# Kernel optimization log

Measured on AMD Instinct MI355X. Metric: run time of the kernel, lower is better.

## Reference

```python
import jax, jax.numpy as jnp
import numpy as np

NUM_BLOCKS = 8
WIDTH = 512
HIDDEN_SIZE_FACTOR = 1
HARD_THRESH_FRAC = 1.0
BLOCK_SIZE = WIDTH // NUM_BLOCKS


def setup_inputs() -> dict:
    key = jax.random.key(0)
    k_x, k1, k2, k3, k4 = jax.random.split(key, 5)
    B, L, P, C = 4, 2048, WIDTH, 8
    bs = BLOCK_SIZE
    hf = HIDDEN_SIZE_FACTOR
    scale = 1.0 / (bs * bs * hf)
    x = jax.random.normal(k_x, (B, L, P, C), dtype=jnp.float32)
    w1 = scale * jax.random.uniform(k1, (2, NUM_BLOCKS, bs, bs * hf), dtype=jnp.float32)
    b1 = scale * jax.random.uniform(k2, (2, NUM_BLOCKS, bs * hf), dtype=jnp.float32)
    w2 = scale * jax.random.uniform(k3, (2, NUM_BLOCKS, bs * hf, bs), dtype=jnp.float32)
    b2 = scale * jax.random.uniform(k4, (2, NUM_BLOCKS, bs), dtype=jnp.float32)
    return {"x": x, "w1": w1, "b1": b1, "w2": w2, "b2": b2}


def _gelu(v):
    # torch nn.GELU default is the exact (erf) variant
    return jax.nn.gelu(v, approximate=False)


def reference(x, w1, b1, w2, b2):
    B, L, P, C = x.shape
    nb, bs = NUM_BLOCKS, BLOCK_SIZE
    # rfft along L (norm='ortho'); complex64
    xf = jnp.fft.rfft(x, axis=1, norm="ortho")          # (B, Lf, P, C)
    Lf = xf.shape[1]
    xf = jnp.transpose(xf, (0, 1, 3, 2))                  # (B, Lf, C, P)
    xf = xf.reshape(B, Lf, C, nb, bs)                     # split P into blocks
    kept = int(Lf * HARD_THRESH_FRAC)
    xr, xi = jnp.real(xf[:, :kept]), jnp.imag(xf[:, :kept])
    # block-diagonal complex 2-layer MLP
    mm = lambda a, w: jnp.einsum("blcni,nio->blcno", a, w)
    o1r = _gelu(mm(xr, w1[0]) - mm(xi, w1[1]) + b1[0])
    o1i = _gelu(mm(xi, w1[0]) + mm(xr, w1[1]) + b1[1])
    o2r = mm(o1r, w2[0]) - mm(o1i, w2[1]) + b2[0]
    o2i = mm(o1i, w2[0]) + mm(o1r, w2[1]) + b2[1]
    # zero-pad the thresholded modes (no-op when kept == Lf)
    pad = Lf - kept
    if pad > 0:
        z = jnp.zeros((B, pad, C, nb, bs), dtype=o2r.dtype)
        o2r = jnp.concatenate([o2r, z], axis=1)
        o2i = jnp.concatenate([o2i, z], axis=1)
    xc = (o2r + 1j * o2i).reshape(B, Lf, C, P)
    out = jnp.fft.irfft(xc, n=L, axis=1, norm="ortho")  # (B, L, C, P)
    out = jnp.transpose(out, (0, 1, 3, 2))               # (B, L, P, C)
    return (out + x).astype(x.dtype)
```

## Files before the change

### kernel.cpp

```cpp
#include <hip/hip_runtime.h>
#include <hip/hip_bf16.h>

typedef unsigned short u16;
typedef unsigned int   u32;
typedef __bf16 bf16x8 __attribute__((ext_vector_type(8)));
typedef float  f32x4  __attribute__((ext_vector_type(4)));
typedef u32    u32x2  __attribute__((ext_vector_type(2)));

#define KPAD 1088
#define SEQ  1104
#define PI_F 3.14159265358979323846f
#define WAVE_FENCE() asm volatile("s_waitcnt lgkmcnt(0)" ::: "memory")

__device__ __forceinline__ u16 f2bf(float f){
    u32 u = __float_as_uint(f);
    return (u16)((u + 0x7FFFu + ((u >> 16) & 1u)) >> 16);
}
__device__ __forceinline__ float bf2f(u16 v){ return __uint_as_float(((u32)v) << 16); }
__device__ __forceinline__ int zmap2(int e){ return e + (e >> 4) + 4*(e >> 8); }

__device__ __forceinline__ int sig(int k){
    k &= 1023;
    int a = (k >> 6) + (((k >> 2) & 15) << 4) + ((k & 3) << 8);
    return zmap2(a);
}

__device__ __forceinline__ float2 cmul(float2 a, float2 b){
    return make_float2(a.x*b.x - a.y*b.y, a.x*b.y + a.y*b.x);
}
__device__ __forceinline__ void fft4v(float2& x0, float2& x1, float2& x2, float2& x3){
    float2 t0 = make_float2(x0.x+x2.x, x0.y+x2.y);
    float2 t1 = make_float2(x0.x-x2.x, x0.y-x2.y);
    float2 t2 = make_float2(x1.x+x3.x, x1.y+x3.y);
    float2 t3 = make_float2(x1.x-x3.x, x1.y-x3.y);
    x0 = make_float2(t0.x+t2.x, t0.y+t2.y);
    x2 = make_float2(t0.x-t2.x, t0.y-t2.y);
    x1 = make_float2(t1.x+t3.y, t1.y-t3.x);
    x3 = make_float2(t1.x-t3.y, t1.y+t3.x);
}
__device__ __forceinline__ void fft16(float2 a[16]){
    #pragma unroll
    for (int u1 = 0; u1 < 4; ++u1) fft4v(a[u1], a[u1+4], a[u1+8], a[u1+12]);
    const float Cq = 0.70710678118654752f;
    const float c1 = 0.92387953251128674f, s1 = 0.38268343236508977f;
    a[5]  = cmul(a[5],  make_float2(c1, -s1));
    a[6]  = cmul(a[6],  make_float2(Cq, -Cq));
    a[7]  = cmul(a[7],  make_float2(s1, -c1));
    a[9]  = cmul(a[9],  make_float2(Cq, -Cq));
    a[10] = cmul(a[10], make_float2(0.0f, -1.0f));
    a[11] = cmul(a[11], make_float2(-Cq, -Cq));
    a[13] = cmul(a[13], make_float2(s1, -c1));
    a[14] = cmul(a[14], make_float2(-Cq, -Cq));
    a[15] = cmul(a[15], make_float2(-c1, s1));
    #pragma unroll
    for (int ja = 0; ja < 4; ++ja) fft4v(a[4*ja], a[4*ja+1], a[4*ja+2], a[4*ja+3]);
}

__device__ __forceinline__ void fft_stepA_wave(float2* Z, int lane){
    #pragma unroll
    for (int i = 0; i < 4; ++i){
        int q = lane + 64*i;
        int u = (q >> 4) & 15;
        float s_, c_;
        __sincosf(-2.0f*PI_F*(float)u*(1.0f/64.0f), &s_, &c_);
        float2 tw1 = make_float2(c_, s_);
        float2 tw2 = cmul(tw1, tw1);
        float2 tw3 = cmul(tw2, tw1);
        float2 x0 = Z[zmap2(q)], x1 = Z[zmap2(q+256)], x2 = Z[zmap2(q+512)], x3 = Z[zmap2(q+768)];
        fft4v(x0, x1, x2, x3);
        Z[zmap2(q)]     = x0;
        Z[zmap2(q+256)] = cmul(x1, tw1);
        Z[zmap2(q+512)] = cmul(x2, tw2);
        Z[zmap2(q+768)] = cmul(x3, tw3);
    }
}
__device__ __forceinline__ void fft_stepB_wave(float2* Z, int lane){
    int nA = lane & 15, jv = lane >> 4;
    float2 a[16];
    #pragma unroll
    for (int u = 0; u < 16; ++u) a[u] = Z[zmap2(nA + 16*u + 256*jv)];
    fft16(a);
    float s_, c_;
    __sincosf(-2.0f*PI_F*(float)(nA*jv)*(1.0f/1024.0f), &s_, &c_);
    float2 tw = make_float2(c_, s_);
    __sincosf(-2.0f*PI_F*(float)nA*(1.0f/256.0f), &s_, &c_);
    float2 st = make_float2(c_, s_);
    #pragma unroll
    for (int ju = 0; ju < 16; ++ju){
        Z[zmap2(nA + 16*ju + 256*jv)] = cmul(a[((ju&3)<<2)|(ju>>2)], tw);
        tw = cmul(tw, st);
    }
}
__device__ __forceinline__ void fft_stepC_wave(float2* Z, int lane){
    int ju = (lane & 63) >> 2, jv = lane & 3;
    float2 a[16];
    #pragma unroll
    for (int nA = 0; nA < 16; ++nA) a[nA] = Z[zmap2(nA + 16*ju + 256*jv)];
    fft16(a);
    #pragma unroll
    for (int kO = 0; kO < 16; ++kO)
        Z[zmap2(kO + 16*ju + 256*jv)] = a[((kO&3)<<2)|(kO>>2)];
}

__global__ __launch_bounds__(256) void prep_w(const float* __restrict__ w1,
                                              const float* __restrict__ w2,
                                              u16* __restrict__ WSW){
    int gid = blockIdx.x * 256 + threadIdx.x;
    int qd = gid >> 12;
    int t  = qd & 1;
    int n  = (qd >> 1) & 7;
    int l  = qd >> 4;
    int rr = gid & 4095;
    int o  = rr >> 6;
    int k  = rr & 63;
    const float* w = l ? w2 : w1;
    WSW[gid] = f2bf(w[((size_t)(t*8 + n)*64 + k)*64 + o]);
}


__device__ __forceinline__ u16 unpack_one(const float2* Zc, int k, int pl, float sf){
    float2 Zk = Zc[sig(k)], Zm = Zc[sig(1024 - k)];
    float sn_, cs_; __sincosf(PI_F*(float)k*(1.0f/1024.0f), &sn_, &cs_);
    float Er=0.5f*(Zk.x+Zm.x), Ei=0.5f*(Zk.y-Zm.y);
    float Dr=0.5f*(Zk.x-Zm.x), Di=0.5f*(Zk.y+Zm.y);
    float Xr = Er + cs_*Di - sn_*Dr;
    float Xi = Ei - sn_*Di - cs_*Dr;
    return f2bf((pl ? Xi : Xr) * sf);
}

__global__ __launch_bounds__(256) void fwd_fft(const float* __restrict__ X,
                                               u16* __restrict__ S){
    __shared__ float2 Zs[4*SEQ];
    int tid = threadIdx.x;
    int blk = blockIdx.x;
    int b = blk >> 10;
    int q = blk & 1023;
    int m8 = q & 7, tq = q >> 3;
    int Q = (tq >> 2)*8 + m8, s4 = tq & 3;
    int col0 = Q*16 + s4*4;
    int p  = col0 >> 3;
    int c0 = col0 & 7;
    int n  = p >> 6, pl_ = p & 63;
    int wave = tid >> 6, lane = tid & 63;

    float2 zz[4][4];
    #pragma unroll
    for (int v = 0; v < 4; ++v){
        int pi = tid + 256*v;
        size_t base = ((size_t)(b*2048 + 2*pi)*512 + p)*8 + c0;
        f32x4 ve = *(const f32x4*)(X + base);
        f32x4 vo = *(const f32x4*)(X + base + 4096);
        #pragma unroll
        for (int s = 0; s < 4; ++s) zz[v][s] = make_float2(ve[s], vo[s]);
    }
    {
        int u = (tid >> 4) & 15;
        float s_, c_;
        __sincosf(-2.0f*PI_F*(float)u*(1.0f/64.0f), &s_, &c_);
        float2 tw1 = make_float2(c_, s_);
        float2 tw2 = cmul(tw1, tw1);
        float2 tw3 = cmul(tw2, tw1);
        #pragma unroll
        for (int s = 0; s < 4; ++s){
            float2 x0 = zz[0][s], x1 = zz[1][s], x2 = zz[2][s], x3 = zz[3][s];
            fft4v(x0, x1, x2, x3);
            float2* Z = Zs + s*SEQ;
            Z[zmap2(tid)]     = x0;
            Z[zmap2(tid+256)] = cmul(x1, tw1);
            Z[zmap2(tid+512)] = cmul(x2, tw2);
            Z[zmap2(tid+768)] = cmul(x3, tw3);
        }
    }
    __syncthreads();
    float2* Z = Zs + wave*SEQ;
    fft_stepB_wave(Z, lane);
    WAVE_FENCE();
    fft_stepC_wave(Z, lane);
    WAVE_FENCE();
    const float sf = 0.02209708691207961f;
    int pl = lane >> 5, tr = lane & 31;
    u16* rp = S + (size_t)((((b*8 + (c0+wave))*8 + n)*2 + pl)*64 + pl_)*KPAD;
    for (int kk = tr*2; kk <= 1024; kk += 64){
        u16 w0 = unpack_one(Z, kk, pl, sf);
        if (kk < 1024){
            u16 w1 = unpack_one(Z, kk+1, pl, sf);
            *(u32*)(rp + kk) = (u32)w0 | ((u32)w1 << 16);
        } else {
            rp[kk] = w0;
        }
    }
}

__device__ __forceinline__ bf16x8 fetchB(const u16* mat, int o64, int k64, bool neg){
    const u32x2* pb = (const u32x2*)(mat + o64*68 + k64);
    u32x2 lo = pb[0], hi = pb[1];
    union { u32 u[4]; bf16x8 v; } bt;
    bt.u[0]=lo.x; bt.u[1]=lo.y; bt.u[2]=hi.x; bt.u[3]=hi.y;
    if (neg){ bt.u[0]^=0x80008000u; bt.u[1]^=0x80008000u; bt.u[2]^=0x80008000u; bt.u[3]^=0x80008000u; }
    return bt.v;
}
__device__ __forceinline__ bf16x8 loadU16x8(const u16* pp){
    union { u32 u[4]; bf16x8 v; } t;
    const u32* qq = (const u32*)pp;
    t.u[0]=qq[0]; t.u[1]=qq[1]; t.u[2]=qq[2]; t.u[3]=qq[3];
    return t.v;
}

__global__ __launch_bounds__(256) void mlp_kernel(const u16* __restrict__ WSW,
                                                  const float* __restrict__ b1,
                                                  const float* __restrict__ b2,
                                                  u16* __restrict__ S){
    __shared__ __align__(16) u16 AT[4][64*68];
    __shared__ __align__(16) u16 AS[8448];
    int tid = threadIdx.x;
    int blk = blockIdx.x;
    int n = blk & 7;
    int rest = blk >> 3;
    int t17 = rest % 17;
    int bc  = rest / 17;
    int b = bc >> 3, c = bc & 7;
    int k0 = t17 << 6;
    int lane = tid & 63, wv = tid >> 6;
    int lane15 = lane & 15, quad = lane >> 4;

    for (int mi = 0; mi < 4; ++mi){
        const u32* src = (const u32*)(WSW + (size_t)(((mi>>1)*8 + n)*2 + (mi&1))*4096);
        u32* dstm = (u32*)AT[mi];
        for (int d = tid; d < 2048; d += 256){
            int o = d >> 5, kk2 = d & 31;
            dstm[o*34 + kk2] = src[d];
        }
    }
    float bb1[8], bb2v[8];
    #pragma unroll
    for (int nb = 0; nb < 8; ++nb){
        int col = nb*16 + lane15;
        int tt = col >> 6, cc = col & 63;
        bb1[nb]  = b1[tt*512 + n*64 + cc];
        bb2v[nb] = b2[tt*512 + n*64 + cc];
    }
    size_t SB = (size_t)(((b*8 + c)*8 + n)*2)*64;
    {
        int rsub = tid & 31;
        for (int rr = tid >> 5; rr < 128; rr += 8){
            const u16* rp = S + (SB + rr)*KPAD + k0;
            u32 w = *(const u32*)(rp + 2*rsub);
            AS[(2*rsub)*132 + rr]   = (u16)(w & 0xFFFFu);
            AS[(2*rsub+1)*132 + rr] = (u16)(w >> 16);
        }
    }
    __syncthreads();
    const u16* arow = AS + (wv*16 + lane15)*132;
    bf16x8 afr[4];
    #pragma unroll
    for (int kb = 0; kb < 4; ++kb)
        afr[kb] = loadU16x8(arow + kb*32 + quad*8);
    f32x4 acc[8];
    #pragma unroll
    for (int nb = 0; nb < 8; ++nb){ acc[nb][0]=bb1[nb]; acc[nb][1]=bb1[nb]; acc[nb][2]=bb1[nb]; acc[nb][3]=bb1[nb]; }
    #pragma unroll
    for (int nb = 0; nb < 8; ++nb){
        int o64 = (nb&3)*16 + lane15;
        #pragma unroll
        for (int kb = 0; kb < 4; ++kb){
            int k64 = (kb&1)*32 + quad*8;
            const u16* mat; bool neg = false;
            if (kb < 2) mat = (nb<4) ? AT[0] : AT[1];
            else { if (nb<4){ mat = AT[1]; neg = true; } else mat = AT[0]; }
            acc[nb] = __builtin_amdgcn_mfma_f32_16x16x32_bf16(afr[kb], fetchB(mat,o64,k64,neg), acc[nb], 0,0,0);
        }
    }
    #pragma unroll
    for (int nb = 0; nb < 8; ++nb){
        #pragma unroll
        for (int r4 = 0; r4 < 4; ++r4){
            float xv = acc[nb][r4];
            float u_ = xv * 0.70710678118f;
            float u2 = u_*u_;
            float pg = 1.0f + u2*(-0.333333333f + u2*(0.1f + u2*(-0.0238095238f)));
            float h  = 0.5f * xv * (1.0f + 1.12837916709551f * u_ * pg);
            AS[(wv*16 + quad*4 + r4)*132 + nb*16 + lane15] = f2bf(h);
        }
    }
    bf16x8 a2[4];
    #pragma unroll
    for (int kb = 0; kb < 4; ++kb)
        a2[kb] = loadU16x8(arow + kb*32 + quad*8);
    f32x4 acc2[8];
    #pragma unroll
    for (int nb = 0; nb < 8; ++nb){ acc2[nb][0]=bb2v[nb]; acc2[nb][1]=bb2v[nb]; acc2[nb][2]=bb2v[nb]; acc2[nb][3]=bb2v[nb]; }
    #pragma unroll
    for (int nb = 0; nb < 8; ++nb){
        int o64 = (nb&3)*16 + lane15;
        #pragma unroll
        for (int kb = 0; kb < 4; ++kb){
            int k64 = (kb&1)*32 + quad*8;
            const u16* mat; bool neg = false;
            if (kb < 2) mat = (nb<4) ? AT[2] : AT[3];
            else { if (nb<4){ mat = AT[3]; neg = true; } else mat = AT[2]; }
            acc2[nb] = __builtin_amdgcn_mfma_f32_16x16x32_bf16(a2[kb], fetchB(mat,o64,k64,neg), acc2[nb], 0,0,0);
        }
    }
    __syncthreads();
    #pragma unroll
    for (int nb = 0; nb < 8; ++nb){
        #pragma unroll
        for (int r4 = 0; r4 < 4; ++r4)
            AS[(nb*16 + lane15)*66 + (wv*16 + quad*4 + r4)] = f2bf(acc2[nb][r4]);
    }
    __syncthreads();
    {
        int rsub = tid & 31;
        int k = k0 + 2*rsub;
        for (int rr = tid >> 5; rr < 128; rr += 8){
            u32 val = *(const u32*)(AS + rr*66 + 2*rsub);
            u16* rp = S + (SB + rr)*KPAD + k0;
            if (k + 1 <= 1024)  *(u32*)(rp + 2*rsub) = val;
            else if (k == 1024) rp[2*rsub] = (u16)(val & 0xFFFFu);
        }
    }
}

__global__ __launch_bounds__(256) void inv_fft(const u16* __restrict__ S,
                                               const float* __restrict__ X,
                                               float* __restrict__ OUT){
    __shared__ float2 Zs[4*SEQ];
    __shared__ float2 ysp[4];
    int tid = threadIdx.x;
    int blk = blockIdx.x;
    int b = blk >> 10;
    int q = blk & 1023;
    int m8 = q & 7, tq = q >> 3;
    int Q = (tq >> 2)*8 + m8, s4 = tq & 3;
    int col0 = Q*16 + s4*4;
    int p  = col0 >> 3;
    int c0 = col0 & 7;
    int n  = p >> 6, pl_ = p & 63;
    int wave = tid >> 6, lane = tid & 63;

    f32x4 xe[4], xo[4];
    #pragma unroll
    for (int i = 0; i < 4; ++i){
        int pi = tid + 256*i;
        size_t base = ((size_t)(b*2048 + 2*pi)*512 + p)*8 + c0;
        xe[i] = *(const f32x4*)(X + base);
        xo[i] = *(const f32x4*)(X + base + 4096);
    }

    float2* Z = Zs + wave*SEQ;
    {
        const u16* rpR = S + (size_t)((((b*8 + (c0+wave))*8 + n)*2 + 0)*64 + pl_)*KPAD;
        const u16* rpI = rpR + (size_t)64*KPAD;
        for (int kk = 2*lane; kk <= 1024; kk += 128){
            u32 wr = *(const u32*)(rpR + kk);
            u32 wi = *(const u32*)(rpI + kk);
            float yr0 = bf2f((u16)(wr & 0xFFFFu));
            float yi0 = bf2f((u16)(wi & 0xFFFFu));
            if (kk == 0)         Z[zmap2(0)] = make_float2(yr0, 0.0f);
            else if (kk == 1024) ysp[wave] = make_float2(yr0, 0.0f);
            else                 Z[zmap2(kk)] = make_float2(yr0, yi0);
            if (kk < 1024){
                float yr1 = bf2f((u16)(wr >> 16));
                float yi1 = bf2f((u16)(wi >> 16));
                Z[zmap2(kk+1)] = make_float2(yr1, yi1);
            }
        }
    }
    WAVE_FENCE();
    for (int i = 0; i < 9; ++i){
        int k = lane + 64*i;
        if (k <= 512){
            float s2_, c2_; __sincosf(PI_F*(float)k*(1.0f/1024.0f), &s2_, &c2_);
            float2 Yk = Z[zmap2(k)];
            float2 Ym = (k == 0) ? ysp[wave] : Z[zmap2(1024 - k)];
            float Ex = 0.5f*(Yk.x + Ym.x);
            float Ey = 0.5f*(Yk.y - Ym.y);
            float Dx = 0.5f*(Yk.x - Ym.x);
            float Dy = 0.5f*(Yk.y + Ym.y);
            float Ox = c2_*Dx - s2_*Dy;
            float Oy = c2_*Dy + s2_*Dx;
            Z[zmap2(k)] = make_float2(Ex - Oy, Ey + Ox);
            if (k > 0 && k < 512)
                Z[zmap2(1024 - k)] = make_float2(Ex + Oy, Ox - Ey);
        }
    }
    WAVE_FENCE();
    fft_stepA_wave(Z, lane);
    WAVE_FENCE();
    fft_stepB_wave(Z, lane);
    WAVE_FENCE();
    fft_stepC_wave(Z, lane);
    __syncthreads();
    const float sc = 0.04419417382415922f;
    #pragma unroll
    for (int i = 0; i < 4; ++i){
        int pi = tid + 256*i;
        int zb = sig(1024 - pi);
        size_t base = ((size_t)(b*2048 + 2*pi)*512 + p)*8 + c0;
        f32x4 oe, oo;
        #pragma unroll
        for (int s = 0; s < 4; ++s){
            float2 r = Zs[s*SEQ + zb];
            oe[s] = r.x*sc + xe[i][s];
            oo[s] = r.y*sc + xo[i][s];
        }
        *(f32x4*)(OUT + base)        = oe;
        *(f32x4*)(OUT + base + 4096) = oo;
    }
}

extern "C" void kernel_launch(void* const* d_in, const int* in_sizes, int n_in,
                              void* d_out, int out_size, void* d_ws, size_t ws_size,
                              hipStream_t stream){
    (void)in_sizes; (void)n_in; (void)out_size; (void)ws_size;
    const float* x  = (const float*)d_in[0];
    const float* w1 = (const float*)d_in[1];
    const float* b1 = (const float*)d_in[2];
    const float* w2 = (const float*)d_in[3];
    const float* b2 = (const float*)d_in[4];
    float* out = (float*)d_out;
    u16* WSW = (u16*)d_ws;
    u16* S1  = (u16*)((char*)d_ws + (1 << 20));

    prep_w<<<dim3(512),  dim3(256), 0, stream>>>(w1, w2, WSW);
    fwd_fft<<<dim3(4096), dim3(256), 0, stream>>>(x, S1);
    mlp_kernel<<<dim3(4352), dim3(256), 0, stream>>>(WSW, b1, b2, S1);
    inv_fft<<<dim3(4096), dim3(256), 0, stream>>>(S1, x, out);
}
```

Baseline: 490.9 us.

## Fuse spectrum load, real-to-complex twist and first FFT stage in registers

The inverse FFT kernel now loads the bf16 spectrum straight into registers and builds the mirrored-bin pairs with cross-lane shuffles instead of going through LDS. The real-to-complex post-processing and the first radix-4 stage also run in registers, with only the stage outputs written to shared memory. This removes two LDS round trips and two wave fences, and hoists the global loads ahead of the residual loads. It also adds a minimum-occupancy hint to launch bounds, which may cap registers and risk spills given the larger register arrays.

```diff
diff --git a/kernel.cpp b/kernel.cpp
--- a/kernel.cpp
+++ b/kernel.cpp
@@ -56,24 +56,6 @@
     for (int ja = 0; ja < 4; ++ja) fft4v(a[4*ja], a[4*ja+1], a[4*ja+2], a[4*ja+3]);
 }
 
-__device__ __forceinline__ void fft_stepA_wave(float2* Z, int lane){
-    #pragma unroll
-    for (int i = 0; i < 4; ++i){
-        int q = lane + 64*i;
-        int u = (q >> 4) & 15;
-        float s_, c_;
-        __sincosf(-2.0f*PI_F*(float)u*(1.0f/64.0f), &s_, &c_);
-        float2 tw1 = make_float2(c_, s_);
-        float2 tw2 = cmul(tw1, tw1);
-        float2 tw3 = cmul(tw2, tw1);
-        float2 x0 = Z[zmap2(q)], x1 = Z[zmap2(q+256)], x2 = Z[zmap2(q+512)], x3 = Z[zmap2(q+768)];
-        fft4v(x0, x1, x2, x3);
-        Z[zmap2(q)]     = x0;
-        Z[zmap2(q+256)] = cmul(x1, tw1);
-        Z[zmap2(q+512)] = cmul(x2, tw2);
-        Z[zmap2(q+768)] = cmul(x3, tw3);
-    }
-}
 __device__ __forceinline__ void fft_stepB_wave(float2* Z, int lane){
     int nA = lane & 15, jv = lane >> 4;
     float2 a[16];
@@ -321,11 +303,10 @@
     }
 }
 
-__global__ __launch_bounds__(256) void inv_fft(const u16* __restrict__ S,
-                                               const float* __restrict__ X,
-                                               float* __restrict__ OUT){
+__global__ __launch_bounds__(256, 4) void inv_fft(const u16* __restrict__ S,
+                                                  const float* __restrict__ X,
+                                                  float* __restrict__ OUT){
     __shared__ float2 Zs[4*SEQ];
-    __shared__ float2 ysp[4];
     int tid = threadIdx.x;
     int blk = blockIdx.x;
     int b = blk >> 10;
@@ -338,6 +319,18 @@
     int n  = p >> 6, pl_ = p & 63;
     int wave = tid >> 6, lane = tid & 63;
 
+    float2* Z = Zs + wave*SEQ;
+
+    const u16* rpR = S + (size_t)((((b*8 + (c0+wave))*8 + n)*2 + 0)*64 + pl_)*KPAD;
+    const u16* rpI = rpR + (size_t)64*KPAD;
+    u32 wR[8], wI[8];
+    #pragma unroll
+    for (int i = 0; i < 8; ++i){
+        wR[i] = *(const u32*)(rpR + 2*lane + 128*i);
+        wI[i] = *(const u32*)(rpI + 2*lane + 128*i);
+    }
+    u16 nyq = rpR[1024];
+
     f32x4 xe[4], xo[4];
     #pragma unroll
     for (int i = 0; i < 4; ++i){
@@ -347,45 +340,100 @@
         xo[i] = *(const f32x4*)(X + base + 4096);
     }
 
-    float2* Z = Zs + wave*SEQ;
-    {
-        const u16* rpR = S + (size_t)((((b*8 + (c0+wave))*8 + n)*2 + 0)*64 + pl_)*KPAD;
-        const u16* rpI = rpR + (size_t)64*KPAD;
-        for (int kk = 2*lane; kk <= 1024; kk += 128){
-            u32 wr = *(const u32*)(rpR + kk);
-            u32 wi = *(const u32*)(rpI + kk);
-            float yr0 = bf2f((u16)(wr & 0xFFFFu));
-            float yi0 = bf2f((u16)(wi & 0xFFFFu));
-            if (kk == 0)         Z[zmap2(0)] = make_float2(yr0, 0.0f);
-            else if (kk == 1024) ysp[wave] = make_float2(yr0, 0.0f);
-            else                 Z[zmap2(kk)] = make_float2(yr0, yi0);
-            if (kk < 1024){
-                float yr1 = bf2f((u16)(wr >> 16));
-                float yi1 = bf2f((u16)(wi >> 16));
-                Z[zmap2(kk+1)] = make_float2(yr1, yi1);
+    float er[8], ei[8], odr[8], odi[8];
+    #pragma unroll
+    for (int i = 0; i < 8; ++i){
+        er[i]  = bf2f((u16)(wR[i] & 0xFFFFu));
+        odr[i] = bf2f((u16)(wR[i] >> 16));
+        ei[i]  = bf2f((u16)(wI[i] & 0xFFFFu));
+        odi[i] = bf2f((u16)(wI[i] >> 16));
+    }
+    float y1024r = bf2f(nyq);
+    if (lane == 0) ei[0] = 0.0f;
+
+    float emr[8], emi[8];
+    {
+        int srcE = (64 - lane) & 63;
+        #pragma unroll
+        for (int i = 0; i < 8; ++i){
+            emr[i] = __shfl(er[7-i], srcE);
+            emi[i] = __shfl(ei[7-i], srcE);
+        }
+        if (lane == 0){
+            emr[0] = y1024r; emi[0] = 0.0f;
+            #pragma unroll
+            for (int i = 1; i < 8; ++i){ emr[i] = er[8-i]; emi[i] = ei[8-i]; }
+        }
+        #pragma unroll
+        for (int i = 0; i < 8; ++i){
+            float s2_, c2_;
+            __sincosf(PI_F*(float)(2*lane + 128*i)*(1.0f/1024.0f), &s2_, &c2_);
+            float Ex = 0.5f*(er[i] + emr[i]), Ey = 0.5f*(ei[i] - emi[i]);
+            float Dx = 0.5f*(er[i] - emr[i]), Dy = 0.5f*(ei[i] + emi[i]);
+            float Ox = c2_*Dx - s2_*Dy,      Oy = c2_*Dy + s2_*Dx;
+            er[i] = Ex - Oy;  ei[i] = Ey + Ox;
+        }
+    }
+    {
+        int srcO = 63 - lane;
+        #pragma unroll
+        for (int i = 0; i < 8; ++i){
+            emr[i] = __shfl(odr[7-i], srcO);
+            emi[i] = __shfl(odi[7-i], srcO);
+        }
+        #pragma unroll
+        for (int i = 0; i < 8; ++i){
+            float s2_, c2_;
+            __sincosf(PI_F*(float)(2*lane + 1 + 128*i)*(1.0f/1024.0f), &s2_, &c2_);
+            float Ex = 0.5f*(odr[i] + emr[i]), Ey = 0.5f*(odi[i] - emi[i]);
+            float Dx = 0.5f*(odr[i] - emr[i]), Dy = 0.5f*(odi[i] + emi[i]);
+            float Ox = c2_*Dx - s2_*Dy,        Oy = c2_*Dy + s2_*Dx;
+            odr[i] = Ex - Oy;  odi[i] = Ey + Ox;
+        }
+    }
+
+    {
+        int u0 = lane >> 3;
+        float su_, cu_;
+        __sincosf(-2.0f*PI_F*(float)u0*(1.0f/64.0f), &su_, &cu_);
+        float2 twa1 = make_float2(cu_, su_);
+        float2 twa2 = cmul(twa1, twa1);
+        float2 twa3 = cmul(twa2, twa1);
+        const float RH = 0.70710678118654752f;
+        float2 rot  = make_float2(RH, -RH);
+        float2 twb1 = cmul(twa1, rot);
+        float2 twb2 = cmul(twb1, twb1);
+        float2 twb3 = cmul(twb2, twb1);
+        #pragma unroll
+        for (int j0 = 0; j0 < 2; ++j0){
+            float2 t1 = j0 ? twb1 : twa1;
+            float2 t2 = j0 ? twb2 : twa2;
+            float2 t3 = j0 ? twb3 : twa3;
+            int qb = 2*lane + 128*j0;
+            {
+                float2 x0 = make_float2(er[j0],   ei[j0]);
+                float2 x1 = make_float2(er[j0+2], ei[j0+2]);
+                float2 x2 = make_float2(er[j0+4], ei[j0+4]);
+                float2 x3 = make_float2(er[j0+6], ei[j0+6]);
+                fft4v(x0, x1, x2, x3);
+                Z[zmap2(qb)]     = x0;
+                Z[zmap2(qb+256)] = cmul(x1, t1);
+                Z[zmap2(qb+512)] = cmul(x2, t2);
+                Z[zmap2(qb+768)] = cmul(x3, t3);
             }
-        }
-    }
-    WAVE_FENCE();
-    for (int i = 0; i < 9; ++i){
-        int k = lane + 64*i;
-        if (k <= 512){
-            float s2_, c2_; __sincosf(PI_F*(float)k*(1.0f/1024.0f), &s2_, &c2_);
-            float2 Yk = Z[zmap2(k)];
-            float2 Ym = (k == 0) ? ysp[wave] : Z[zmap2(1024 - k)];
-            float Ex = 0.5f*(Yk.x + Ym.x);
-            float Ey = 0.5f*(Yk.y - Ym.y);
-            float Dx = 0.5f*(Yk.x - Ym.x);
-            float Dy = 0.5f*(Yk.y + Ym.y);
-            float Ox = c2_*Dx - s2_*Dy;
-            float Oy = c2_*Dy + s2_*Dx;
-            Z[zmap2(k)] = make_float2(Ex - Oy, Ey + Ox);
-            if (k > 0 && k < 512)
-                Z[zmap2(1024 - k)] = make_float2(Ex + Oy, Ox - Ey);
-        }
-    }
-    WAVE_FENCE();
-    fft_stepA_wave(Z, lane);
+            {
+                float2 x0 = make_float2(odr[j0],   odi[j0]);
+                float2 x1 = make_float2(odr[j0+2], odi[j0+2]);
+                float2 x2 = make_float2(odr[j0+4], odi[j0+4]);
+                float2 x3 = make_float2(odr[j0+6], odi[j0+6]);
+                fft4v(x0, x1, x2, x3);
+                Z[zmap2(qb+1)]   = x0;
+                Z[zmap2(qb+257)] = cmul(x1, t1);
+                Z[zmap2(qb+513)] = cmul(x2, t2);
+                Z[zmap2(qb+769)] = cmul(x3, t3);
+            }
+        }
+    }
     WAVE_FENCE();
     fft_stepB_wave(Z, lane);
     WAVE_FENCE();
```

Result: slower. 501.6 us (+2.2%).
